# Kernel optimization log

Measured on AMD Instinct MI355X. Metric: run time of the kernel, lower is better.

Reference implementation:

```python
import jax, jax.numpy as jnp
import numpy as np

NUM_HEADS = 16

def setup_inputs() -> dict:
    key = jax.random.key(0)
    k1, k2, k3 = jax.random.split(key, 3)
    B, S, H = 2, 2048, 1024
    hidden_states = jax.random.normal(k1, (B, S, H), dtype=jnp.float32)
    # nn.Linear default init scale ~ 1/sqrt(fan_in); keep magnitudes sane
    w_qkv = jax.random.normal(k2, (3 * H, H), dtype=jnp.float32) * (1.0 / np.sqrt(H))
    w_o = jax.random.normal(k3, (H, H), dtype=jnp.float32) * (1.0 / np.sqrt(H))
    return {"hidden_states": hidden_states, "w_qkv": w_qkv, "w_o": w_o}

def reference(hidden_states, w_qkv, w_o):
    B, S, H = hidden_states.shape
    nh = NUM_HEADS
    hd = H // nh
    scale = 1.0 / np.sqrt(hd)
    # fused QKV projection: [B,S,3H]
    qkv = jnp.einsum('bsh,oh->bso', hidden_states, w_qkv)
    qkv = qkv.reshape(B, S, 3, nh, hd)
    q = qkv[:, :, 0].transpose(0, 2, 1, 3)  # [B, nh, S, hd]
    k = qkv[:, :, 1].transpose(0, 2, 1, 3)
    v = qkv[:, :, 2].transpose(0, 2, 1, 3)
    # scaled dot-product attention (math identical to the online-softmax path)
    scores = jnp.einsum('bhqd,bhkd->bhqk', q, k) * scale
    probs = jax.nn.softmax(scores, axis=-1)
    attn = jnp.einsum('bhqk,bhkd->bhqd', probs, v)  # [B, nh, S, hd]
    attn = attn.transpose(0, 2, 1, 3).reshape(B, S, H)
    out = jnp.einsum('bsh,oh->bso', attn, w_o)
    return out
```

## Files before the change

### kernel.cpp

```cpp
#include <hip/hip_runtime.h>

using f32x4 = __attribute__((ext_vector_type(4))) float;
using s16x8 = __attribute__((ext_vector_type(8))) short;
using u16x8 = __attribute__((ext_vector_type(8))) unsigned short;
using u16x4 = __attribute__((ext_vector_type(4))) unsigned short;
using u32x2 = __attribute__((ext_vector_type(2))) unsigned int;

__device__ __forceinline__ unsigned short f2bf(float f) {
  union { float f; unsigned u; } v; v.f = f;
  return (unsigned short)((v.u + 0x7FFFu + ((v.u >> 16) & 1u)) >> 16);
}

__device__ __forceinline__ unsigned pk2bf(float a, float b) {
#if __has_builtin(__builtin_amdgcn_cvt_pk_bf16_f32)
  typedef __bf16 bf2 __attribute__((ext_vector_type(2)));
  union { bf2 v; unsigned u; } c;
  c.v = __builtin_amdgcn_cvt_pk_bf16_f32(a, b);
  return c.u;
#else
  return (unsigned)f2bf(a) | ((unsigned)f2bf(b) << 16);
#endif
}

__device__ __forceinline__ f32x4 fzero4() {
  f32x4 z; z[0] = 0.f; z[1] = 0.f; z[2] = 0.f; z[3] = 0.f; return z;
}

__device__ __forceinline__ void gl_lds16(const void* g, void* l) {
  __builtin_amdgcn_global_load_lds(
      (const __attribute__((address_space(1))) unsigned int*)g,
      (__attribute__((address_space(3))) unsigned int*)l, 16, 0, 0);
}

__global__ __launch_bounds__(256) void cvt_bf16(const float* __restrict__ h,
                                                const float* __restrict__ wq,
                                                const float* __restrict__ wo,
                                                unsigned short* __restrict__ dst) {
  const int blk = blockIdx.x;
  const float* src;
  if (blk < 2048) src = h;
  else if (blk < 3584) src = wq - 4194304;
  else src = wo - (4194304 + 3145728);
  const size_t i = (size_t)blk * 2048 + threadIdx.x * 8;
  f32x4 a0 = *(const f32x4*)(src + i);
  f32x4 a1 = *(const f32x4*)(src + i + 4);
  u32x2 v0, v1;
  v0[0] = pk2bf(a0[0], a0[1]); v0[1] = pk2bf(a0[2], a0[3]);
  v1[0] = pk2bf(a1[0], a1[1]); v1[1] = pk2bf(a1[2], a1[3]);
  *(u32x2*)(dst + i) = v0;
  *(u32x2*)(dst + i + 4) = v1;
}

template <int CMODE>
__global__ __launch_bounds__(256) void gemm_bt(const unsigned short* __restrict__ A,
                                               const unsigned short* __restrict__ B,
                                               void* __restrict__ Cp,
                                               void* __restrict__ Vgp,
                                               int M, int N, int K) {
  __shared__ unsigned short As[128 * 64];
  __shared__ unsigned short Bs[128 * 64];
  const int t = threadIdx.x;
  const int lane = t & 63, wid = t >> 6;
  const int l15 = lane & 15, quad = lane >> 4;
  const int bm = blockIdx.x * 128, bn = blockIdx.y * 128;
  const int wm = (wid >> 1) * 64, wn = (wid & 1) * 64;
  const int wbase = t & ~63;

  f32x4 acc[4][4];
#pragma unroll
  for (int i = 0; i < 4; ++i)
#pragma unroll
    for (int j = 0; j < 4; ++j) acc[i][j] = fzero4();

  for (int k0 = 0; k0 < K; k0 += 64) {
    __syncthreads();
#pragma unroll
    for (int i = 0; i < 4; ++i) {
      const int dc = t + i * 256;
      const int row = dc >> 3, cp = dc & 7;
      const int cl = cp ^ (row & 7);
      gl_lds16(A + (size_t)(bm + row) * K + k0 + cl * 8, &As[(size_t)(i * 256 + wbase) * 8]);
      gl_lds16(B + (size_t)(bn + row) * K + k0 + cl * 8, &Bs[(size_t)(i * 256 + wbase) * 8]);
    }
    __syncthreads();
#pragma unroll
    for (int c = 0; c < 2; ++c) {
      s16x8 af[4], bf[4];
#pragma unroll
      for (int mt = 0; mt < 4; ++mt) {
        const int row = wm + mt * 16 + l15;
        af[mt] = *(const s16x8*)&As[row * 64 + (((c * 4 + quad) ^ (l15 & 7)) * 8)];
      }
#pragma unroll
      for (int nt = 0; nt < 4; ++nt) {
        const int row = wn + nt * 16 + l15;
        bf[nt] = *(const s16x8*)&Bs[row * 64 + (((c * 4 + quad) ^ (l15 & 7)) * 8)];
      }
#pragma unroll
      for (int mt = 0; mt < 4; ++mt)
#pragma unroll
        for (int nt = 0; nt < 4; ++nt)
          acc[mt][nt] = __builtin_amdgcn_mfma_f32_16x16x32_bf16(af[mt], bf[nt], acc[mt][nt], 0, 0, 0);
    }
  }

  if (CMODE == 2 && bn >= 2048) {
#pragma unroll
    for (int mt = 0; mt < 4; ++mt)
#pragma unroll
      for (int nt = 0; nt < 4; ++nt) {
        const int row0 = bm + wm + mt * 16 + quad * 4;
        const int c = bn + wn + nt * 16 + l15 - 2048;
        const int b = row0 >> 11, s = row0 & 2047;
        u32x2 ov;
        ov[0] = pk2bf(acc[mt][nt][0], acc[mt][nt][1]);
        ov[1] = pk2bf(acc[mt][nt][2], acc[mt][nt][3]);
        *(u32x2*)&((unsigned short*)Vgp)[(size_t)b * (1024 * 2048) + (size_t)c * 2048 + s] = ov;
      }
    return;
  }

  const float qscale = (CMODE == 2 && bn < 1024) ? 0.18033688011112042f : 1.0f;
#pragma unroll
  for (int mt = 0; mt < 4; ++mt)
#pragma unroll
    for (int nt = 0; nt < 4; ++nt)
#pragma unroll
      for (int r = 0; r < 4; ++r) {
        const int row = bm + wm + mt * 16 + quad * 4 + r;
        const int col = bn + wn + nt * 16 + l15;
        if (CMODE == 0)
          ((float*)Cp)[(size_t)row * N + col] = acc[mt][nt][r];
        else
          ((unsigned short*)Cp)[(size_t)row * 2048 + col] = f2bf(acc[mt][nt][r] * qscale);
      }
}

__global__ __launch_bounds__(256) void fattn(const unsigned short* __restrict__ qk,
                                             const unsigned short* __restrict__ vg,
                                             unsigned short* __restrict__ attn) {
  constexpr int S = 2048, H = 1024, LD = 2048, HD = 64;
  __shared__ unsigned short Ks[2][64 * 64];
  __shared__ unsigned short Vt[2][64 * 64];
  __shared__ unsigned short Pn[4][32][72];

  const int t = threadIdx.x, lane = t & 63, wid = t >> 6;
  const int l15 = lane & 15, quad = lane >> 4;
  const int qt = blockIdx.x, h = blockIdx.y, b = blockIdx.z;
  const unsigned short* qbase = qk + (size_t)b * S * LD;
  const unsigned short* kbase = qbase + 1024 + h * HD;
  const unsigned short* vbase = vg + ((size_t)b * 16 + h) * HD * S;
  const int qrow0 = qt * 128;
  const int wbase = t & ~63;

  s16x8 qf[2][2];
#pragma unroll
  for (int nt = 0; nt < 2; ++nt)
#pragma unroll
    for (int c = 0; c < 2; ++c)
      qf[nt][c] = *(const s16x8*)(qbase + (size_t)(qrow0 + wid * 32 + nt * 16 + l15) * LD +
                                  h * HD + c * 32 + quad * 8);

  s16x8 ones;
#pragma unroll
  for (int j = 0; j < 8; ++j) ones[j] = (short)0x3F80;

  f32x4 o[4][2], lacc[2];
#pragma unroll
  for (int i = 0; i < 4; ++i)
#pragma unroll
    for (int j = 0; j < 2; ++j) o[i][j] = fzero4();
  lacc[0] = fzero4(); lacc[1] = fzero4();

  auto stage = [&](int kt, int bu) {
#pragma unroll
    for (int i = 0; i < 2; ++i) {
      const int pos = t + i * 256;
      const int row = pos >> 3, s = pos & 7;
      const int clog = s ^ (row & 7);
      gl_lds16(kbase + (size_t)(kt * 64 + row) * LD + clog * 8,
               &Ks[bu][(size_t)(i * 256 + wbase) * 8]);
      gl_lds16(vbase + (size_t)row * S + kt * 64 + clog * 8,
               &Vt[bu][(size_t)(i * 256 + wbase) * 8]);
    }
  };

  stage(0, 0);
  __syncthreads();

  for (int kt = 0; kt < S / 64; ++kt) {
    const int cur = kt & 1;
    if (kt < S / 64 - 1) stage(kt + 1, cur ^ 1);

    const unsigned short* K = Ks[cur];
    const unsigned short* V = Vt[cur];

    f32x4 st[4][2];
#pragma unroll
    for (int i = 0; i < 4; ++i)
#pragma unroll
      for (int j = 0; j < 2; ++j) st[i][j] = fzero4();
#pragma unroll
    for (int c = 0; c < 2; ++c) {
      s16x8 kf[4];
#pragma unroll
      for (int mt = 0; mt < 4; ++mt)
        kf[mt] = *(const s16x8*)&K[(mt * 16 + l15) * 64 + ((c * 4 + quad) ^ (l15 & 7)) * 8];
#pragma unroll
      for (int mt = 0; mt < 4; ++mt)
#pragma unroll
        for (int nt = 0; nt < 2; ++nt)
          st[mt][nt] = __builtin_amdgcn_mfma_f32_16x16x32_bf16(kf[mt], qf[nt][c], st[mt][nt], 0, 0, 0);
    }

#pragma unroll
    for (int mt = 0; mt < 4; ++mt)
#pragma unroll
      for (int nt = 0; nt < 2; ++nt)
#pragma unroll
        for (int r = 0; r < 4; ++r) st[mt][nt][r] = __builtin_amdgcn_exp2f(st[mt][nt][r]);

#pragma unroll
    for (int mt = 0; mt < 4; ++mt)
#pragma unroll
      for (int nt = 0; nt < 2; ++nt) {
        u32x2 pk;
        pk[0] = pk2bf(st[mt][nt][0], st[mt][nt][1]);
        pk[1] = pk2bf(st[mt][nt][2], st[mt][nt][3]);
        *(u32x2*)&Pn[wid][nt * 16 + l15][mt * 16 + quad * 4] = pk;
      }

#pragma unroll
    for (int c = 0; c < 2; ++c) {
      s16x8 pf[2];
#pragma unroll
      for (int nt = 0; nt < 2; ++nt) {
        pf[nt] = *(const s16x8*)&Pn[wid][nt * 16 + l15][c * 32 + quad * 8];
        lacc[nt] = __builtin_amdgcn_mfma_f32_16x16x32_bf16(ones, pf[nt], lacc[nt], 0, 0, 0);
      }
#pragma unroll
      for (int mt = 0; mt < 4; ++mt) {
        s16x8 vf = *(const s16x8*)&V[(mt * 16 + l15) * 64 + ((c * 4 + quad) ^ (l15 & 7)) * 8];
#pragma unroll
        for (int nt = 0; nt < 2; ++nt)
          o[mt][nt] = __builtin_amdgcn_mfma_f32_16x16x32_bf16(vf, pf[nt], o[mt][nt], 0, 0, 0);
      }
    }

    __syncthreads();
  }

#pragma unroll
  for (int nt = 0; nt < 2; ++nt) {
    const float inv = 1.f / lacc[nt][0];
    const int row = b * S + qrow0 + wid * 32 + nt * 16 + l15;
#pragma unroll
    for (int mt = 0; mt < 4; ++mt) {
      u32x2 ov;
      ov[0] = pk2bf(o[mt][nt][0] * inv, o[mt][nt][1] * inv);
      ov[1] = pk2bf(o[mt][nt][2] * inv, o[mt][nt][3] * inv);
      *(u32x2*)&attn[(size_t)row * H + h * HD + mt * 16 + quad * 4] = ov;
    }
  }
}

extern "C" void kernel_launch(void* const* d_in, const int* in_sizes, int n_in,
                              void* d_out, int out_size, void* d_ws, size_t ws_size,
                              hipStream_t stream) {
  const float* hidden = (const float*)d_in[0];
  const float* w_qkv = (const float*)d_in[1];
  const float* w_o = (const float*)d_in[2];
  float* out = (float*)d_out;

  constexpr int B = 2, S = 2048, H = 1024;
  constexpr int M = B * S;

  unsigned short* hbf = (unsigned short*)d_ws;
  unsigned short* wqbf = hbf + 4194304;
  unsigned short* wobf = wqbf + 3145728;
  unsigned short* qkbuf = wobf + 1048576;
  unsigned short* vg = qkbuf + (size_t)M * 2048;
  unsigned short* attn = hbf;

  dim3 blk(256);
  cvt_bf16<<<4096, blk, 0, stream>>>(hidden, w_qkv, w_o, hbf);
  gemm_bt<2><<<dim3(M / 128, (3 * H) / 128), blk, 0, stream>>>(
      hbf, wqbf, (void*)qkbuf, (void*)vg, M, 3 * H, H);
  fattn<<<dim3(S / 128, 16, B), blk, 0, stream>>>(qkbuf, vg, attn);
  gemm_bt<0><<<dim3(M / 128, H / 128), blk, 0, stream>>>(
      attn, wobf, (void*)out, nullptr, M, H, H);
}
```

Measured before the change: 187.6 us.

## Double-buffer GEMM LDS tiles with BK=32 to overlap loads and MFMA

Replaces the single 128x64 LDS tile loop in gemm_bt with two 128x32 buffers, prefetching the next K-slice into the alternate buffer while MFMAs run on the current one. This drops one barrier per iteration and hides global-to-LDS latency. The XOR swizzle is removed, so the row stride becomes 32 shorts (64 bytes), which may cause LDS bank conflicts on fragment reads. The loop also runs twice as many iterations, each with half the MFMA work.

```diff
diff --git a/kernel.cpp b/kernel.cpp
--- a/kernel.cpp
+++ b/kernel.cpp
@@ -57,8 +57,8 @@
                                                void* __restrict__ Cp,
                                                void* __restrict__ Vgp,
                                                int M, int N, int K) {
-  __shared__ unsigned short As[128 * 64];
-  __shared__ unsigned short Bs[128 * 64];
+  __shared__ unsigned short As[2][128 * 32];
+  __shared__ unsigned short Bs[2][128 * 32];
   const int t = threadIdx.x;
   const int lane = t & 63, wid = t >> 6;
   const int l15 = lane & 15, quad = lane >> 4;
@@ -72,36 +72,38 @@
 #pragma unroll
     for (int j = 0; j < 4; ++j) acc[i][j] = fzero4();
 
-  for (int k0 = 0; k0 < K; k0 += 64) {
+  auto stage = [&](int k0, int bu) {
+#pragma unroll
+    for (int i = 0; i < 2; ++i) {
+      const int pos = t + i * 256;
+      const int row = pos >> 2, ck = (pos & 3) * 8;
+      gl_lds16(A + (size_t)(bm + row) * K + k0 + ck, &As[bu][(size_t)(i * 256 + wbase) * 8]);
+      gl_lds16(B + (size_t)(bn + row) * K + k0 + ck, &Bs[bu][(size_t)(i * 256 + wbase) * 8]);
+    }
+  };
+
+  stage(0, 0);
+  __syncthreads();
+
+  const int NT = K >> 5;
+  for (int kt = 0; kt < NT; ++kt) {
+    const int cur = kt & 1;
+    if (kt + 1 < NT) stage((kt + 1) * 32, cur ^ 1);
+
+    s16x8 af[4], bf[4];
+#pragma unroll
+    for (int mt = 0; mt < 4; ++mt)
+      af[mt] = *(const s16x8*)&As[cur][(wm + mt * 16 + l15) * 32 + quad * 8];
+#pragma unroll
+    for (int nt = 0; nt < 4; ++nt)
+      bf[nt] = *(const s16x8*)&Bs[cur][(wn + nt * 16 + l15) * 32 + quad * 8];
+#pragma unroll
+    for (int mt = 0; mt < 4; ++mt)
+#pragma unroll
+      for (int nt = 0; nt < 4; ++nt)
+        acc[mt][nt] = __builtin_amdgcn_mfma_f32_16x16x32_bf16(af[mt], bf[nt], acc[mt][nt], 0, 0, 0);
+
     __syncthreads();
-#pragma unroll
-    for (int i = 0; i < 4; ++i) {
-      const int dc = t + i * 256;
-      const int row = dc >> 3, cp = dc & 7;
-      const int cl = cp ^ (row & 7);
-      gl_lds16(A + (size_t)(bm + row) * K + k0 + cl * 8, &As[(size_t)(i * 256 + wbase) * 8]);
-      gl_lds16(B + (size_t)(bn + row) * K + k0 + cl * 8, &Bs[(size_t)(i * 256 + wbase) * 8]);
-    }
-    __syncthreads();
-#pragma unroll
-    for (int c = 0; c < 2; ++c) {
-      s16x8 af[4], bf[4];
-#pragma unroll
-      for (int mt = 0; mt < 4; ++mt) {
-        const int row = wm + mt * 16 + l15;
-        af[mt] = *(const s16x8*)&As[row * 64 + (((c * 4 + quad) ^ (l15 & 7)) * 8)];
-      }
-#pragma unroll
-      for (int nt = 0; nt < 4; ++nt) {
-        const int row = wn + nt * 16 + l15;
-        bf[nt] = *(const s16x8*)&Bs[row * 64 + (((c * 4 + quad) ^ (l15 & 7)) * 8)];
-      }
-#pragma unroll
-      for (int mt = 0; mt < 4; ++mt)
-#pragma unroll
-        for (int nt = 0; nt < 4; ++nt)
-          acc[mt][nt] = __builtin_amdgcn_mfma_f32_16x16x32_bf16(af[mt], bf[nt], acc[mt][nt], 0, 0, 0);
-    }
   }
 
   if (CMODE == 2 && bn >= 2048) {
```

Result: slower. 193.1 us (+2.9%).
